# Kernel tuning notes

Hardware: AMD Instinct MI355X
Metric: run time of the kernel (lower is better)

## Reference

```python
import jax, jax.numpy as jnp
import numpy as np

NUM_HEADS = 16

def setup_inputs() -> dict:
    key = jax.random.key(0)
    k1, k2, k3 = jax.random.split(key, 3)
    B, N, C = 2, 2048, 1024
    x = jax.random.normal(k1, (B, N, C), dtype=jnp.float32)
    w_qkv = jax.random.normal(k2, (C, 3 * C), dtype=jnp.float32) * (C ** -0.5)
    w_proj = jax.random.normal(k3, (C, C), dtype=jnp.float32) * (C ** -0.5)
    b_proj = jnp.zeros((C,), dtype=jnp.float32)
    return {"x": x, "w_qkv": w_qkv, "w_proj": w_proj, "b_proj": b_proj}

def reference(x, w_qkv, w_proj, b_proj):
    B, N, C = x.shape
    H = NUM_HEADS
    D = C // H
    scale = D ** -0.5
    qkv = x @ w_qkv                               # [B,N,3C]
    qkv = qkv.reshape(B, N, 3, H, D).transpose(2, 0, 3, 1, 4)  # [3,B,H,N,D]
    q, k, v = qkv[0] * scale, qkv[1], qkv[2]
    attn = jnp.einsum('bhnd,bhmd->bhnm', q, k)    # [B,H,N,N]
    attn = jax.nn.softmax(attn, axis=-1)
    out = jnp.einsum('bhnm,bhmd->bhnd', attn, v)  # [B,H,N,D]
    out = out.transpose(0, 2, 1, 3).reshape(B, N, C)
    return out @ w_proj + b_proj
```

## Files before the change

kernel.cpp:

```cpp
#include <hip/hip_runtime.h>

typedef unsigned short ushort_t;
typedef __attribute__((ext_vector_type(8))) short short8;
typedef __attribute__((ext_vector_type(4))) float f32x4;

#define AS1 __attribute__((address_space(1)))
#define AS3 __attribute__((address_space(3)))

__device__ __forceinline__ ushort_t f2bf(float f) {
    union { float f; unsigned u; } v; v.f = f;
    unsigned r = v.u + 0x7fffu + ((v.u >> 16) & 1u);
    return (ushort_t)(r >> 16);
}

__device__ __forceinline__ unsigned pack_bf16_pair(float a, float b) {
    unsigned ua = __float_as_uint(a) + 0x8000u;
    unsigned ub = __float_as_uint(b) + 0x8000u;
    return __builtin_amdgcn_perm(ub, ua, 0x07060302u);
}

__device__ __forceinline__ void gl_lds16(const ushort_t* g, ushort_t* lds_base) {
    __builtin_amdgcn_global_load_lds((const AS1 unsigned int*)(size_t)g,
                                     (AS3 unsigned int*)lds_base, 16, 0, 0);
}

__device__ __forceinline__ void transpose_body(
    const float* __restrict__ in, ushort_t* __restrict__ out,
    int K0, int N0, int n, int k0)
{
    ushort_t vals[32];
#pragma unroll
    for (int kk = 0; kk < 32; kk++)
        vals[kk] = f2bf(in[(size_t)(k0 + kk) * N0 + n]);
#pragma unroll
    for (int c = 0; c < 4; c++) {
        short8 v;
#pragma unroll
        for (int e = 0; e < 8; e++) v[e] = (short)vals[c * 8 + e];
        *(short8*)&out[(size_t)n * K0 + k0 + c * 8] = v;
    }
}

__global__ __launch_bounds__(256) void prep_kernel(
    const float* __restrict__ x, const float* __restrict__ wqkv,
    const float* __restrict__ wproj,
    ushort_t* __restrict__ Xb, ushort_t* __restrict__ WqkvT,
    ushort_t* __restrict__ WpT)
{
    const int blk = blockIdx.x, t = threadIdx.x;
    if (blk < 2048) {
        int idx = (blk * 256 + t) * 8;
        float4 a = *(const float4*)&x[idx];
        float4 b = *(const float4*)&x[idx + 4];
        short8 v;
        v[0] = (short)f2bf(a.x); v[1] = (short)f2bf(a.y);
        v[2] = (short)f2bf(a.z); v[3] = (short)f2bf(a.w);
        v[4] = (short)f2bf(b.x); v[5] = (short)f2bf(b.y);
        v[6] = (short)f2bf(b.z); v[7] = (short)f2bf(b.w);
        *(short8*)&Xb[idx] = v;
    } else if (blk < 2048 + 384) {
        int i = blk - 2048;
        transpose_body(wqkv, WqkvT, 1024, 3072, (i % 12) * 256 + t, (i / 12) * 32);
    } else {
        int i = blk - 2432;
        transpose_body(wproj, WpT, 1024, 1024, (i % 4) * 256 + t, (i / 4) * 32);
    }
}

template<int JT>
__device__ __forceinline__ void mfma_gemm_core(
    const ushort_t* __restrict__ A, const ushort_t* __restrict__ Bt,
    int bm, int bn, int w, int lane,
    ushort_t* Atile, ushort_t* Btile, f32x4 acc[4][JT])
{
    const int K = 1024;
    const int wy = w >> 1, wx = w & 1;
    const int lrow8 = lane >> 3;
    const int srcoct = (lane & 7) ^ (lrow8 & 7);
    const int fr = lane & 15, fo = lane >> 4;

    for (int k0 = 0; k0 < K; k0 += 64) {
        __syncthreads();
#pragma unroll
        for (int it = 0; it < 4; it++) {
            int L = w * 4 + it;
            int r = 8 * L + lrow8;
            gl_lds16(A + (size_t)(bm + r) * K + k0 + srcoct * 8, Atile + L * 512);
        }
#pragma unroll
        for (int it = 0; it < JT; it++) {
            int L = w * JT + it;
            int r = 8 * L + lrow8;
            gl_lds16(Bt + (size_t)(bn + r) * K + k0 + srcoct * 8, Btile + L * 512);
        }
        __syncthreads();
#pragma unroll
        for (int s = 0; s < 2; s++) {
            short8 af[4], bf[JT];
#pragma unroll
            for (int i = 0; i < 4; i++) {
                int m = wy * 64 + i * 16 + fr;
                af[i] = *(const short8*)&Atile[m * 64 + (((s * 4 + fo) ^ (m & 7)) * 8)];
            }
#pragma unroll
            for (int j = 0; j < JT; j++) {
                int n = wx * (JT * 16) + j * 16 + fr;
                bf[j] = *(const short8*)&Btile[n * 64 + (((s * 4 + fo) ^ (n & 7)) * 8)];
            }
#pragma unroll
            for (int i = 0; i < 4; i++)
#pragma unroll
                for (int j = 0; j < JT; j++)
                    acc[i][j] = __builtin_amdgcn_mfma_f32_16x16x32_bf16(
                        af[i], bf[j], acc[i][j], 0, 0, 0);
        }
    }
}

__global__ __launch_bounds__(256) void qkv_gemm_kernel(
    const ushort_t* __restrict__ Xb, const ushort_t* __restrict__ WqkvT,
    ushort_t* __restrict__ Qb, ushort_t* __restrict__ Kb, ushort_t* __restrict__ Vtb)
{
    __shared__ __align__(16) ushort_t Atile[128 * 64];
    __shared__ __align__(16) ushort_t Btile[128 * 64];
    const int t = threadIdx.x, w = t >> 6, lane = t & 63;
    const int bm = blockIdx.y * 128, bn = blockIdx.x * 128;

    f32x4 acc[4][4];
#pragma unroll
    for (int i = 0; i < 4; i++)
#pragma unroll
        for (int j = 0; j < 4; j++) acc[i][j] = (f32x4){0.f, 0.f, 0.f, 0.f};

    mfma_gemm_core<4>(Xb, WqkvT, bm, bn, w, lane, Atile, Btile, acc);

    const int wy = w >> 1, wx = w & 1;
    const int colbase = bn + wx * 64 + (lane & 15);
    const int rowbase = bm + wy * 64 + (lane >> 4) * 4;
#pragma unroll
    for (int i = 0; i < 4; i++) {
#pragma unroll
        for (int r = 0; r < 4; r++) {
            int row = rowbase + i * 16 + r;
            int b = row >> 11, n = row & 2047;
#pragma unroll
            for (int j = 0; j < 4; j++) {
                int col = colbase + j * 16;
                float v = acc[i][j][r];
                int which = col >> 10;
                int hc = col & 1023;
                int h = hc >> 6, d = hc & 63;
                int bh = b * 16 + h;
                if (which == 0)
                    Qb[((size_t)bh * 2048 + n) * 64 + d] = f2bf(v * 0.125f);
                else if (which == 1)
                    Kb[((size_t)bh * 2048 + n) * 64 + d] = f2bf(v);
                else
                    Vtb[((size_t)bh * 64 + d) * 2048 + n] = f2bf(v);
            }
        }
    }
}

__global__ __launch_bounds__(256, 4) void attn_kernel(
    const ushort_t* __restrict__ Q, const ushort_t* __restrict__ K,
    const ushort_t* __restrict__ Vt, ushort_t* __restrict__ O)
{
    __shared__ __align__(16) ushort_t QPs[64 * 64];
    __shared__ __align__(16) ushort_t Ks [64 * 64];
    __shared__ __align__(16) ushort_t Vts[64 * 64];
    __shared__ float l_lds[64];

    const int q0 = blockIdx.x * 64;
    const int bh = blockIdx.y;
    const int t = threadIdx.x, w = t >> 6, lane = t & 63;
    const int lrow8 = lane >> 3;
    const int srcoct = (lane & 7) ^ (lrow8 & 7);
    const int fr = lane & 15, fo = lane >> 4;

    const ushort_t* Qh = Q  + (size_t)bh * 2048 * 64;
    const ushort_t* Kh = K  + (size_t)bh * 2048 * 64;
    const ushort_t* Vh = Vt + (size_t)bh * 64 * 2048;

#pragma unroll
    for (int it = 0; it < 2; it++) {
        int L = w * 2 + it;
        int r = 8 * L + lrow8;
        gl_lds16(Qh + (size_t)(q0 + r) * 64 + srcoct * 8, QPs + L * 512);
    }
    if (t < 64) l_lds[t] = 0.f;
    __syncthreads();

    short8 qf[4][2];
#pragma unroll
    for (int jq = 0; jq < 4; jq++)
#pragma unroll
        for (int s = 0; s < 2; s++) {
            int m = jq * 16 + fr;
            qf[jq][s] = *(const short8*)&QPs[m * 64 + (((s * 4 + fo) ^ (m & 7)) * 8)];
        }

    f32x4 o_acc[4];
    float l_part[4];
#pragma unroll
    for (int j = 0; j < 4; j++) { o_acc[j] = (f32x4){0.f, 0.f, 0.f, 0.f}; l_part[j] = 0.f; }

    const ushort_t* kp[2];
    const ushort_t* vp[2];
#pragma unroll
    for (int it = 0; it < 2; it++) {
        int r = 8 * (w * 2 + it) + lrow8;
        kp[it] = Kh + (size_t)r * 64   + srcoct * 8;
        vp[it] = Vh + (size_t)r * 2048 + srcoct * 8;
    }

    for (int kt = 0; kt < 32; kt++) {
        __syncthreads();
#pragma unroll
        for (int it = 0; it < 2; it++) {
            gl_lds16(kp[it], Ks  + (w * 2 + it) * 512);  kp[it] += 64 * 64;
            gl_lds16(vp[it], Vts + (w * 2 + it) * 512);  vp[it] += 64;
        }
        __syncthreads();

        f32x4 s_acc[4];
#pragma unroll
        for (int j = 0; j < 4; j++) s_acc[j] = (f32x4){0.f, 0.f, 0.f, 0.f};
#pragma unroll
        for (int s = 0; s < 2; s++) {
            int mk = 16 * w + fr;
            short8 kf = *(const short8*)&Ks[mk * 64 + (((s * 4 + fo) ^ (mk & 7)) * 8)];
#pragma unroll
            for (int jq = 0; jq < 4; jq++)
                s_acc[jq] = __builtin_amdgcn_mfma_f32_16x16x32_bf16(
                    kf, qf[jq][s], s_acc[jq], 0, 0, 0);
        }

#pragma unroll
        for (int jq = 0; jq < 4; jq++) {
            float p0 = __expf(s_acc[jq][0]);
            float p1 = __expf(s_acc[jq][1]);
            float p2 = __expf(s_acc[jq][2]);
            float p3 = __expf(s_acc[jq][3]);
            l_part[jq] += (p0 + p1) + (p2 + p3);
            unsigned d0 = pack_bf16_pair(p0, p1);
            unsigned d1 = pack_bf16_pair(p2, p3);
            int q   = jq * 16 + fr;
            int oct = 2 * w + (fo >> 1);
            int addr = q * 64 + ((oct ^ (q & 7)) * 8) + (fo & 1) * 4;
            *(uint2*)&QPs[addr] = make_uint2(d0, d1);
        }
        __syncthreads();

#pragma unroll
        for (int s = 0; s < 2; s++) {
            int mq = 16 * w + fr;
            short8 pf = *(const short8*)&QPs[mq * 64 + (((s * 4 + fo) ^ (mq & 7)) * 8)];
#pragma unroll
            for (int jd = 0; jd < 4; jd++) {
                int nd = jd * 16 + fr;
                short8 vf = *(const short8*)&Vts[nd * 64 + (((s * 4 + fo) ^ (nd & 7)) * 8)];
                o_acc[jd] = __builtin_amdgcn_mfma_f32_16x16x32_bf16(
                    pf, vf, o_acc[jd], 0, 0, 0);
            }
        }
    }

#pragma unroll
    for (int jq = 0; jq < 4; jq++)
        atomicAdd(&l_lds[jq * 16 + fr], l_part[jq]);
    __syncthreads();

    const int b = bh >> 4, h = bh & 15;
#pragma unroll
    for (int r = 0; r < 4; r++) {
        int qrow = 16 * w + fo * 4 + r;
        float inv = 1.f / l_lds[qrow];
        int row = b * 2048 + q0 + qrow;
#pragma unroll
        for (int jd = 0; jd < 4; jd++) {
            int col = h * 64 + jd * 16 + fr;
            O[(size_t)row * 1024 + col] = f2bf(o_acc[jd][r] * inv);
        }
    }
}

__global__ __launch_bounds__(256) void proj_gemm_kernel(
    const ushort_t* __restrict__ Ao, const ushort_t* __restrict__ WpT,
    const float* __restrict__ bias, float* __restrict__ out)
{
    __shared__ __align__(16) ushort_t Atile[128 * 64];
    __shared__ __align__(16) ushort_t Btile[64 * 64];
    const int t = threadIdx.x, w = t >> 6, lane = t & 63;
    const int bm = blockIdx.y * 128, bn = blockIdx.x * 64;

    f32x4 acc[4][2];
#pragma unroll
    for (int i = 0; i < 4; i++)
#pragma unroll
        for (int j = 0; j < 2; j++) acc[i][j] = (f32x4){0.f, 0.f, 0.f, 0.f};

    mfma_gemm_core<2>(Ao, WpT, bm, bn, w, lane, Atile, Btile, acc);

    const int wy = w >> 1, wx = w & 1;
    const int colbase = bn + wx * 32 + (lane & 15);
    const int rowbase = bm + wy * 64 + (lane >> 4) * 4;
#pragma unroll
    for (int i = 0; i < 4; i++) {
#pragma unroll
        for (int r = 0; r < 4; r++) {
            int row = rowbase + i * 16 + r;
#pragma unroll
            for (int j = 0; j < 2; j++) {
                int col = colbase + j * 16;
                out[(size_t)row * 1024 + col] = acc[i][j][r] + bias[col];
            }
        }
    }
}

extern "C" void kernel_launch(void* const* d_in, const int* in_sizes, int n_in,
                              void* d_out, int out_size, void* d_ws, size_t ws_size,
                              hipStream_t stream) {
    const float* x      = (const float*)d_in[0];
    const float* w_qkv  = (const float*)d_in[1];
    const float* w_proj = (const float*)d_in[2];
    const float* b_proj = (const float*)d_in[3];
    float* out = (float*)d_out;

    char* ws = (char*)d_ws;
    ushort_t* Xb    = (ushort_t*)(ws);
    ushort_t* WqkvT = (ushort_t*)(ws + ((size_t)8  << 20));
    ushort_t* WpT   = (ushort_t*)(ws + ((size_t)14 << 20));
    ushort_t* Qb    = (ushort_t*)(ws + ((size_t)16 << 20));
    ushort_t* Kb    = (ushort_t*)(ws + ((size_t)24 << 20));
    ushort_t* Vtb   = (ushort_t*)(ws + ((size_t)32 << 20));
    ushort_t* Aob   = (ushort_t*)(ws + ((size_t)40 << 20));

    prep_kernel<<<2560, 256, 0, stream>>>(x, w_qkv, w_proj, Xb, WqkvT, WpT);
    qkv_gemm_kernel<<<dim3(24, 32), 256, 0, stream>>>(Xb, WqkvT, Qb, Kb, Vtb);
    attn_kernel<<<dim3(32, 32), 256, 0, stream>>>(Qb, Kb, Vtb, Aob);
    proj_gemm_kernel<<<dim3(16, 32), 256, 0, stream>>>(Aob, WpT, b_proj, out);
}
```

Before: 218.9 us.

## Keep P in registers for PV MFMA, use exp2 with folded log2e scale

The attention kernel no longer writes the softmax probabilities to LDS and syncs. Each wave now feeds its own P fragments straight from registers into the PV MFMA, using zero-padded half-K operands, and keeps 16 partial O accumulators. The partials are reduced across waves through LDS atomics at the end. The Q scale now folds in log2(e) so a native exp2 can replace expf. The QKV epilogue also writes V with packed vector stores. This trades one barrier and an LDS round trip per key tile for twice the MFMA work on half-empty operands, more registers (occupancy hint lowered from 4 to 3), and an atomic reduction at the end.

```diff
diff --git a/kernel.cpp b/kernel.cpp
--- a/kernel.cpp
+++ b/kernel.cpp
@@ -6,6 +6,8 @@
 
 #define AS1 __attribute__((address_space(1)))
 #define AS3 __attribute__((address_space(3)))
+
+#define EXP2F(x) __builtin_amdgcn_exp2f(x)
 
 __device__ __forceinline__ ushort_t f2bf(float f) {
     union { float f; unsigned u; } v; v.f = f;
@@ -23,6 +25,8 @@
     __builtin_amdgcn_global_load_lds((const AS1 unsigned int*)(size_t)g,
                                      (AS3 unsigned int*)lds_base, 16, 0, 0);
 }
+
+#define QSCALE 0.18033688011112042f
 
 __device__ __forceinline__ void transpose_body(
     const float* __restrict__ in, ushort_t* __restrict__ out,
@@ -139,37 +143,48 @@
     const int rowbase = bm + wy * 64 + (lane >> 4) * 4;
 #pragma unroll
     for (int i = 0; i < 4; i++) {
-#pragma unroll
-        for (int r = 0; r < 4; r++) {
-            int row = rowbase + i * 16 + r;
-            int b = row >> 11, n = row & 2047;
-#pragma unroll
-            for (int j = 0; j < 4; j++) {
-                int col = colbase + j * 16;
-                float v = acc[i][j][r];
-                int which = col >> 10;
+        int n0 = rowbase + i * 16;
+        int b = n0 >> 11, n = n0 & 2047;
+#pragma unroll
+        for (int j = 0; j < 4; j++) {
+            int col = colbase + j * 16;
+            f32x4 a = acc[i][j];
+            if (col < 1024) {
+                int h = col >> 6, d = col & 63;
+                size_t base = ((size_t)(b * 16 + h) * 2048 + n) * 64 + d;
+#pragma unroll
+                for (int r = 0; r < 4; r++)
+                    Qb[base + (size_t)r * 64] = f2bf(a[r] * QSCALE);
+            } else if (col < 2048) {
                 int hc = col & 1023;
                 int h = hc >> 6, d = hc & 63;
-                int bh = b * 16 + h;
-                if (which == 0)
-                    Qb[((size_t)bh * 2048 + n) * 64 + d] = f2bf(v * 0.125f);
-                else if (which == 1)
-                    Kb[((size_t)bh * 2048 + n) * 64 + d] = f2bf(v);
-                else
-                    Vtb[((size_t)bh * 64 + d) * 2048 + n] = f2bf(v);
-            }
-        }
-    }
-}
-
-__global__ __launch_bounds__(256, 4) void attn_kernel(
+                size_t base = ((size_t)(b * 16 + h) * 2048 + n) * 64 + d;
+#pragma unroll
+                for (int r = 0; r < 4; r++)
+                    Kb[base + (size_t)r * 64] = f2bf(a[r]);
+            } else {
+                int hc = col & 1023;
+                int h = hc >> 6, d = hc & 63;
+                unsigned d0 = pack_bf16_pair(a[0], a[1]);
+                unsigned d1 = pack_bf16_pair(a[2], a[3]);
+                *(uint2*)&Vtb[((size_t)(b * 16 + h) * 64 + d) * 2048 + n] =
+                    make_uint2(d0, d1);
+            }
+        }
+    }
+}
+
+__global__ __launch_bounds__(256, 3) void attn_kernel(
     const ushort_t* __restrict__ Q, const ushort_t* __restrict__ K,
     const ushort_t* __restrict__ Vt, ushort_t* __restrict__ O)
 {
-    __shared__ __align__(16) ushort_t QPs[64 * 64];
-    __shared__ __align__(16) ushort_t Ks [64 * 64];
-    __shared__ __align__(16) ushort_t Vts[64 * 64];
+    __shared__ __align__(16) ushort_t Qs[64 * 64];
+    __shared__ __align__(16) ushort_t KV[2 * 64 * 64];
     __shared__ float l_lds[64];
+
+    ushort_t* Ks   = KV;
+    ushort_t* Vts  = KV + 64 * 64;
+    float*    Ored = (float*)KV;
 
     const int q0 = blockIdx.x * 64;
     const int bh = blockIdx.y;
@@ -186,7 +201,7 @@
     for (int it = 0; it < 2; it++) {
         int L = w * 2 + it;
         int r = 8 * L + lrow8;
-        gl_lds16(Qh + (size_t)(q0 + r) * 64 + srcoct * 8, QPs + L * 512);
+        gl_lds16(Qh + (size_t)(q0 + r) * 64 + srcoct * 8, Qs + L * 512);
     }
     if (t < 64) l_lds[t] = 0.f;
     __syncthreads();
@@ -197,13 +212,17 @@
 #pragma unroll
         for (int s = 0; s < 2; s++) {
             int m = jq * 16 + fr;
-            qf[jq][s] = *(const short8*)&QPs[m * 64 + (((s * 4 + fo) ^ (m & 7)) * 8)];
-        }
-
-    f32x4 o_acc[4];
+            qf[jq][s] = *(const short8*)&Qs[m * 64 + (((s * 4 + fo) ^ (m & 7)) * 8)];
+        }
+
+    f32x4 o_acc[4][4];
     float l_part[4];
 #pragma unroll
-    for (int j = 0; j < 4; j++) { o_acc[j] = (f32x4){0.f, 0.f, 0.f, 0.f}; l_part[j] = 0.f; }
+    for (int jd = 0; jd < 4; jd++)
+#pragma unroll
+        for (int jq = 0; jq < 4; jq++) o_acc[jd][jq] = (f32x4){0.f, 0.f, 0.f, 0.f};
+#pragma unroll
+    for (int j = 0; j < 4; j++) l_part[j] = 0.f;
 
     const ushort_t* kp[2];
     const ushort_t* vp[2];
@@ -236,34 +255,36 @@
                     kf, qf[jq][s], s_acc[jq], 0, 0, 0);
         }
 
+        short8 pb[4];
 #pragma unroll
         for (int jq = 0; jq < 4; jq++) {
-            float p0 = __expf(s_acc[jq][0]);
-            float p1 = __expf(s_acc[jq][1]);
-            float p2 = __expf(s_acc[jq][2]);
-            float p3 = __expf(s_acc[jq][3]);
+            float p0 = EXP2F(s_acc[jq][0]);
+            float p1 = EXP2F(s_acc[jq][1]);
+            float p2 = EXP2F(s_acc[jq][2]);
+            float p3 = EXP2F(s_acc[jq][3]);
             l_part[jq] += (p0 + p1) + (p2 + p3);
-            unsigned d0 = pack_bf16_pair(p0, p1);
-            unsigned d1 = pack_bf16_pair(p2, p3);
-            int q   = jq * 16 + fr;
-            int oct = 2 * w + (fo >> 1);
-            int addr = q * 64 + ((oct ^ (q & 7)) * 8) + (fo & 1) * 4;
-            *(uint2*)&QPs[addr] = make_uint2(d0, d1);
-        }
-        __syncthreads();
-
-#pragma unroll
-        for (int s = 0; s < 2; s++) {
-            int mq = 16 * w + fr;
-            short8 pf = *(const short8*)&QPs[mq * 64 + (((s * 4 + fo) ^ (mq & 7)) * 8)];
-#pragma unroll
-            for (int jd = 0; jd < 4; jd++) {
-                int nd = jd * 16 + fr;
-                short8 vf = *(const short8*)&Vts[nd * 64 + (((s * 4 + fo) ^ (nd & 7)) * 8)];
-                o_acc[jd] = __builtin_amdgcn_mfma_f32_16x16x32_bf16(
-                    pf, vf, o_acc[jd], 0, 0, 0);
-            }
-        }
+            uint4 pu;
+            pu.x = pack_bf16_pair(p0, p1);
+            pu.y = pack_bf16_pair(p2, p3);
+            pu.z = 0u; pu.w = 0u;
+            pb[jq] = __builtin_bit_cast(short8, pu);
+        }
+
+        short8 va[4];
+#pragma unroll
+        for (int jd = 0; jd < 4; jd++) {
+            int nd = jd * 16 + fr;
+            int oct = (2 * w + (fo >> 1)) ^ (nd & 7);
+            uint2 v2 = *(const uint2*)&Vts[nd * 64 + oct * 8 + (fo & 1) * 4];
+            uint4 vu; vu.x = v2.x; vu.y = v2.y; vu.z = 0u; vu.w = 0u;
+            va[jd] = __builtin_bit_cast(short8, vu);
+        }
+#pragma unroll
+        for (int jd = 0; jd < 4; jd++)
+#pragma unroll
+            for (int jq = 0; jq < 4; jq++)
+                o_acc[jd][jq] = __builtin_amdgcn_mfma_f32_16x16x32_bf16(
+                    va[jd], pb[jq], o_acc[jd][jq], 0, 0, 0);
     }
 
 #pragma unroll
@@ -271,17 +292,41 @@
         atomicAdd(&l_lds[jq * 16 + fr], l_part[jq]);
     __syncthreads();
 
-    const int b = bh >> 4, h = bh & 15;
-#pragma unroll
-    for (int r = 0; r < 4; r++) {
-        int qrow = 16 * w + fo * 4 + r;
-        float inv = 1.f / l_lds[qrow];
-        int row = b * 2048 + q0 + qrow;
-#pragma unroll
-        for (int jd = 0; jd < 4; jd++) {
-            int col = h * 64 + jd * 16 + fr;
-            O[(size_t)row * 1024 + col] = f2bf(o_acc[jd][r] * inv);
-        }
+#pragma unroll
+    for (int i = 0; i < 4; i++)
+        ((f32x4*)Ored)[t * 4 + i] = (f32x4){0.f, 0.f, 0.f, 0.f};
+    __syncthreads();
+
+#pragma unroll
+    for (int jd = 0; jd < 4; jd++)
+#pragma unroll
+        for (int jq = 0; jq < 4; jq++)
+#pragma unroll
+            for (int r = 0; r < 4; r++) {
+                int d = jd * 16 + fo * 4 + r;
+                int q = jq * 16 + fr;
+                atomicAdd(&Ored[d * 64 + (q ^ ((d & 7) << 2))], o_acc[jd][jq][r]);
+            }
+    __syncthreads();
+
+    {
+        int q  = t >> 2, dg = t & 3;
+        float inv = 1.f / l_lds[q];
+        int row = (bh >> 4) * 2048 + q0 + q;
+        int col = (bh & 15) * 64 + dg * 16;
+        unsigned dw[8];
+#pragma unroll
+        for (int i = 0; i < 8; i++) {
+            int d0 = dg * 16 + 2 * i, d1 = d0 + 1;
+            float v0 = Ored[d0 * 64 + (q ^ ((d0 & 7) << 2))] * inv;
+            float v1 = Ored[d1 * 64 + (q ^ ((d1 & 7) << 2))] * inv;
+            dw[i] = pack_bf16_pair(v0, v1);
+        }
+        uint4 lo, hi;
+        lo.x = dw[0]; lo.y = dw[1]; lo.z = dw[2]; lo.w = dw[3];
+        hi.x = dw[4]; hi.y = dw[5]; hi.z = dw[6]; hi.w = dw[7];
+        *(uint4*)&O[(size_t)row * 1024 + col]     = lo;
+        *(uint4*)&O[(size_t)row * 1024 + col + 8] = hi;
     }
 }
 
```

Result: slower. 298.8 us (+36.5%).

## Double-buffer K/V tiles in attention, use exp2 with prescaled Q, vectorize V stores

Applied to the files above, without the earlier changes.

The attention kernel now keeps two K/V LDS buffers and prefetches the next tile while computing on the current one, removing one barrier per iteration so global loads overlap compute. Q is prescaled by scale*log2(e) so the softmax can use the hardware exp2 instruction instead of __expf. The QKV epilogue is restructured so V^T writes are packed 4-wide, and occupancy is lowered to 3 blocks per SM because of the larger LDS. Reusing the QPs buffer and LDS slots across the overlapped loads relies on the remaining barrier ordering, and the last iteration issues a redundant wrap-around prefetch.

```diff
diff --git a/kernel.cpp b/kernel.cpp
--- a/kernel.cpp
+++ b/kernel.cpp
@@ -6,6 +6,8 @@
 
 #define AS1 __attribute__((address_space(1)))
 #define AS3 __attribute__((address_space(3)))
+
+#define EXP2F(x) __builtin_amdgcn_exp2f(x)
 
 __device__ __forceinline__ ushort_t f2bf(float f) {
     union { float f; unsigned u; } v; v.f = f;
@@ -23,6 +25,8 @@
     __builtin_amdgcn_global_load_lds((const AS1 unsigned int*)(size_t)g,
                                      (AS3 unsigned int*)lds_base, 16, 0, 0);
 }
+
+#define QSCALE 0.18033688011112042f
 
 __device__ __forceinline__ void transpose_body(
     const float* __restrict__ in, ushort_t* __restrict__ out,
@@ -139,36 +143,43 @@
     const int rowbase = bm + wy * 64 + (lane >> 4) * 4;
 #pragma unroll
     for (int i = 0; i < 4; i++) {
-#pragma unroll
-        for (int r = 0; r < 4; r++) {
-            int row = rowbase + i * 16 + r;
-            int b = row >> 11, n = row & 2047;
-#pragma unroll
-            for (int j = 0; j < 4; j++) {
-                int col = colbase + j * 16;
-                float v = acc[i][j][r];
-                int which = col >> 10;
+        int n0 = rowbase + i * 16;
+        int b = n0 >> 11, n = n0 & 2047;
+#pragma unroll
+        for (int j = 0; j < 4; j++) {
+            int col = colbase + j * 16;
+            f32x4 a = acc[i][j];
+            if (col < 1024) {
+                int h = col >> 6, d = col & 63;
+                size_t base = ((size_t)(b * 16 + h) * 2048 + n) * 64 + d;
+#pragma unroll
+                for (int r = 0; r < 4; r++)
+                    Qb[base + (size_t)r * 64] = f2bf(a[r] * QSCALE);
+            } else if (col < 2048) {
                 int hc = col & 1023;
                 int h = hc >> 6, d = hc & 63;
-                int bh = b * 16 + h;
-                if (which == 0)
-                    Qb[((size_t)bh * 2048 + n) * 64 + d] = f2bf(v * 0.125f);
-                else if (which == 1)
-                    Kb[((size_t)bh * 2048 + n) * 64 + d] = f2bf(v);
-                else
-                    Vtb[((size_t)bh * 64 + d) * 2048 + n] = f2bf(v);
-            }
-        }
-    }
-}
-
-__global__ __launch_bounds__(256, 4) void attn_kernel(
+                size_t base = ((size_t)(b * 16 + h) * 2048 + n) * 64 + d;
+#pragma unroll
+                for (int r = 0; r < 4; r++)
+                    Kb[base + (size_t)r * 64] = f2bf(a[r]);
+            } else {
+                int hc = col & 1023;
+                int h = hc >> 6, d = hc & 63;
+                unsigned d0 = pack_bf16_pair(a[0], a[1]);
+                unsigned d1 = pack_bf16_pair(a[2], a[3]);
+                *(uint2*)&Vtb[((size_t)(b * 16 + h) * 64 + d) * 2048 + n] =
+                    make_uint2(d0, d1);
+            }
+        }
+    }
+}
+
+__global__ __launch_bounds__(256, 3) void attn_kernel(
     const ushort_t* __restrict__ Q, const ushort_t* __restrict__ K,
     const ushort_t* __restrict__ Vt, ushort_t* __restrict__ O)
 {
     __shared__ __align__(16) ushort_t QPs[64 * 64];
-    __shared__ __align__(16) ushort_t Ks [64 * 64];
-    __shared__ __align__(16) ushort_t Vts[64 * 64];
+    __shared__ __align__(16) ushort_t KV[2][2 * 64 * 64];
     __shared__ float l_lds[64];
 
     const int q0 = blockIdx.x * 64;
@@ -185,8 +196,10 @@
 #pragma unroll
     for (int it = 0; it < 2; it++) {
         int L = w * 2 + it;
-        int r = 8 * L + lrow8;
+        int r = 16 * w + 8 * it + lrow8;
         gl_lds16(Qh + (size_t)(q0 + r) * 64 + srcoct * 8, QPs + L * 512);
+        gl_lds16(Kh + (size_t)r * 64 + srcoct * 8,        &KV[0][L * 512]);
+        gl_lds16(Vh + (size_t)r * 2048 + srcoct * 8,      &KV[0][4096 + L * 512]);
     }
     if (t < 64) l_lds[t] = 0.f;
     __syncthreads();
@@ -205,23 +218,20 @@
 #pragma unroll
     for (int j = 0; j < 4; j++) { o_acc[j] = (f32x4){0.f, 0.f, 0.f, 0.f}; l_part[j] = 0.f; }
 
-    const ushort_t* kp[2];
-    const ushort_t* vp[2];
-#pragma unroll
-    for (int it = 0; it < 2; it++) {
-        int r = 8 * (w * 2 + it) + lrow8;
-        kp[it] = Kh + (size_t)r * 64   + srcoct * 8;
-        vp[it] = Vh + (size_t)r * 2048 + srcoct * 8;
-    }
-
+    int cur = 0;
     for (int kt = 0; kt < 32; kt++) {
         __syncthreads();
+        const int u = (kt + 1) & 31;
+        const int nxt = cur ^ 1;
 #pragma unroll
         for (int it = 0; it < 2; it++) {
-            gl_lds16(kp[it], Ks  + (w * 2 + it) * 512);  kp[it] += 64 * 64;
-            gl_lds16(vp[it], Vts + (w * 2 + it) * 512);  vp[it] += 64;
-        }
-        __syncthreads();
+            int L = w * 2 + it;
+            int r = 16 * w + 8 * it + lrow8;
+            gl_lds16(Kh + ((size_t)u * 64 + r) * 64 + srcoct * 8, &KV[nxt][L * 512]);
+            gl_lds16(Vh + (size_t)r * 2048 + u * 64 + srcoct * 8, &KV[nxt][4096 + L * 512]);
+        }
+        const ushort_t* Ks  = KV[cur];
+        const ushort_t* Vts = KV[cur] + 4096;
 
         f32x4 s_acc[4];
 #pragma unroll
@@ -238,10 +248,10 @@
 
 #pragma unroll
         for (int jq = 0; jq < 4; jq++) {
-            float p0 = __expf(s_acc[jq][0]);
-            float p1 = __expf(s_acc[jq][1]);
-            float p2 = __expf(s_acc[jq][2]);
-            float p3 = __expf(s_acc[jq][3]);
+            float p0 = EXP2F(s_acc[jq][0]);
+            float p1 = EXP2F(s_acc[jq][1]);
+            float p2 = EXP2F(s_acc[jq][2]);
+            float p3 = EXP2F(s_acc[jq][3]);
             l_part[jq] += (p0 + p1) + (p2 + p3);
             unsigned d0 = pack_bf16_pair(p0, p1);
             unsigned d1 = pack_bf16_pair(p2, p3);
@@ -264,6 +274,7 @@
                     pf, vf, o_acc[jd], 0, 0, 0);
             }
         }
+        cur = nxt;
     }
 
 #pragma unroll
```

Measured after the change: 221.9 us. Within noise of the previous version (+1.4%).
